# Kernel optimization log

Measured on AMD Instinct MI355X. Metric: run time of the kernel, lower is better.

The kernel has to match this reference:

```python
import jax, jax.numpy as jnp
import numpy as np

B, S, HID, NH, K = 4, 1500, 1024, 16, 64
DH = HID // NH  # 64


def _rel_bias(pos_emb, length):
    # pos_emb: [2K+1, d]; Shaw-style relative position embedding lookup -> [S, S, d]
    kk = (pos_emb.shape[0] - 1) // 2
    idx = jnp.arange(length)
    dist = jnp.clip(idx[None, :] - idx[:, None], -kk, kk) + kk
    return pos_emb[dist]


def setup_inputs() -> dict:
    key = jax.random.key(0)
    ks = jax.random.split(key, 12)
    sq = 1.0 / np.sqrt(HID)
    inp = {
        "query": jax.random.normal(ks[0], (B, S, HID), jnp.float32),
        "key": jax.random.normal(ks[1], (B, S, HID), jnp.float32),
        "value": jax.random.normal(ks[2], (B, S, HID), jnp.float32),
        # per-head QKV projections stacked over heads: [NH, HID, DH]
        "Wq": jax.random.normal(ks[3], (NH, HID, DH), jnp.float32) * sq,
        "bq": jnp.zeros((NH, DH), jnp.float32),
        "Wk": jax.random.normal(ks[4], (NH, HID, DH), jnp.float32) * sq,
        "bk": jnp.zeros((NH, DH), jnp.float32),
        "Wv": jax.random.normal(ks[5], (NH, HID, DH), jnp.float32) * sq,
        "bv": jnp.zeros((NH, DH), jnp.float32),
        # relative position tables [2K+1, DH]
        "pos_k": jax.random.normal(ks[6], (2 * K + 1, DH), jnp.float32) * 0.1,
        "pos_v": jax.random.normal(ks[7], (2 * K + 1, DH), jnp.float32) * 0.1,
        # output projection
        "W_fc": jax.random.normal(ks[8], (HID, HID), jnp.float32) * sq,
        "b_fc": jnp.zeros((HID,), jnp.float32),
    }
    return inp


def reference(query, key, value, Wq, bq, Wk, bk, Wv, bv, pos_k, pos_v, W_fc, b_fc):
    seq = query.shape[1]
    k_bias = _rel_bias(pos_k, seq)  # [S, S, DH]
    v_bias = _rel_bias(pos_v, seq)  # [S, S, DH]

    # batched per-head projections: [B, NH, S, DH]
    q = jnp.einsum('bsh,nhd->bnsd', query, Wq) + bq[None, :, None, :]
    k = jnp.einsum('bsh,nhd->bnsd', key, Wk) + bk[None, :, None, :]
    v = jnp.einsum('bsh,nhd->bnsd', value, Wv) + bv[None, :, None, :]

    attn_1 = jnp.einsum('bnqd,bnkd->bnqk', q, k)
    attn_2 = jnp.einsum('bnqd,qkd->bnqk', q, k_bias)  # Shaw relative key bias
    scores = (attn_1 + attn_2) / jnp.sqrt(jnp.float32(DH))
    w = jax.nn.softmax(scores, axis=-1)  # [B, NH, S, S]

    values_1 = jnp.einsum('bnqk,bnkd->bnqd', w, v)
    values_2 = jnp.einsum('bnqk,qkd->bnqd', w, v_bias)  # Shaw relative value bias
    heads = values_1 + values_2  # [B, NH, S, DH]

    # concat heads in head order -> [B, S, HID]
    hidden = jnp.transpose(heads, (0, 2, 1, 3)).reshape(query.shape[0], seq, -1)
    return hidden @ W_fc + b_fc
```

## Files before the change

kernel.cpp:

```cpp
#include <hip/hip_runtime.h>
#include <stdint.h>

typedef unsigned short u16;
typedef __attribute__((ext_vector_type(8))) short bf16x8;
typedef __attribute__((ext_vector_type(4))) float f32x4;

#define MFMA16(a, b, c) __builtin_amdgcn_mfma_f32_16x16x32_bf16(a, b, c, 0, 0, 0)

__device__ __forceinline__ u16 f2bf(float x) {
  union { float f; uint32_t u; } v; v.f = x;
  uint32_t r = (v.u + 0x7FFFu + ((v.u >> 16) & 1u)) >> 16;
  return (u16)r;
}
__device__ __forceinline__ float bf2f(u16 h) {
  union { uint32_t u; float f; } v; v.u = ((uint32_t)h) << 16; return v.f;
}
__device__ __forceinline__ uint cvt_pk_bf16(float a, float b) {
  uint r;
  asm("v_cvt_pk_bf16_f32 %0, %1, %2" : "=v"(r) : "v"(a), "v"(b));
  return r;
}
__device__ __forceinline__ void gll16(const void* g, void* s) {
  __builtin_amdgcn_global_load_lds((const __attribute__((address_space(1))) unsigned int*)g,
                                   (__attribute__((address_space(3))) unsigned int*)s, 16, 0, 0);
}


__global__ __launch_bounds__(256) void pack_x_kernel(const float* __restrict__ q,
                                                     const float* __restrict__ k,
                                                     const float* __restrict__ v,
                                                     u16* __restrict__ X) {
  const float* src = blockIdx.z == 0 ? q : (blockIdx.z == 1 ? k : v);
  u16* dst = X + (size_t)blockIdx.z * (6016UL * 1024UL);
  size_t idx = (size_t)blockIdx.x * 1024 + (size_t)threadIdx.x * 4;
  float4 f = *(const float4*)(src + idx);
  uint2 o;
  o.x = cvt_pk_bf16(f.x, f.y);
  o.y = cvt_pk_bf16(f.z, f.w);
  *(uint2*)(dst + idx) = o;
}

__global__ __launch_bounds__(256) void pack_w_kernel(const float* __restrict__ Wq,
                                                     const float* __restrict__ Wk,
                                                     const float* __restrict__ Wv,
                                                     const float* __restrict__ Wfc,
                                                     const float* __restrict__ bq,
                                                     const float* __restrict__ bk,
                                                     const float* __restrict__ bv,
                                                     const float* __restrict__ posk,
                                                     const float* __restrict__ posv,
                                                     u16* __restrict__ Wt,
                                                     u16* __restrict__ Wfct,
                                                     float* __restrict__ biascat,
                                                     u16* __restrict__ poskbf,
                                                     u16* __restrict__ posvT) {
  __shared__ float tile[64][65];
  const int bi = blockIdx.x;
  if (bi == 1024) {
    for (int i = threadIdx.x; i < 1024; i += 256) {
      biascat[i] = bq[i]; biascat[1024 + i] = bk[i]; biascat[2048 + i] = bv[i];
    }
    for (int i = threadIdx.x; i < 144 * 64; i += 256) {
      int r = i >> 6;
      poskbf[i] = (r < 129) ? f2bf(posk[i]) : (u16)0;
    }
    const int d = threadIdx.x & 63, rr = threadIdx.x >> 6;
#pragma unroll
    for (int j = 0; j < 34; ++j) {
      const int r = rr * 34 + j;
      posvT[d * 136 + r] = (r < 129) ? f2bf(posv[(size_t)r * 64 + d]) : (u16)0;
    }
    return;
  }
  const int r = threadIdx.x >> 2, c0 = (threadIdx.x & 3) * 16;
  const float* src;
  u16* outp;
  if (bi < 768) {
    const int z = bi >> 8, rem = bi & 255, n = rem >> 4, h0 = (rem & 15) * 64;
    const float* W = z == 0 ? Wq : (z == 1 ? Wk : Wv);
    src = W + (size_t)n * 65536 + (size_t)(h0 + r) * 64 + c0;
    outp = Wt + (size_t)z * (1024UL * 1024UL) + (size_t)(n * 64 + r) * 1024 + h0 + c0;
  } else {
    const int t = bi - 768;
    const int i0 = (t & 15) * 64, o0 = (t >> 4) * 64;
    src = Wfc + (size_t)(i0 + r) * 1024 + o0 + c0;
    outp = Wfct + (size_t)(o0 + r) * 1024 + i0 + c0;
  }
#pragma unroll
  for (int j = 0; j < 16; j += 4) {
    float4 f = *(const float4*)(src + j);
    tile[r][c0 + j] = f.x; tile[r][c0 + j + 1] = f.y;
    tile[r][c0 + j + 2] = f.z; tile[r][c0 + j + 3] = f.w;
  }
  __syncthreads();
#pragma unroll
  for (int j = 0; j < 16; ++j) outp[j] = f2bf(tile[c0 + j][r]);
}

__global__ __launch_bounds__(256) void vtrans_kernel(const u16* __restrict__ qkv,
                                                     u16* __restrict__ Vt) {
  const size_t ZS = 4UL * 16 * 1536 * 64;
  __shared__ u16 t[64][72];
  const int bh = blockIdx.x & 63, s0 = (blockIdx.x >> 6) * 64;
  const u16* src = qkv + 2 * ZS + (size_t)bh * (1536UL * 64UL) + (size_t)s0 * 64;
  const int r = threadIdx.x >> 2, c0 = (threadIdx.x & 3) * 16;
  *(uint4*)&t[r][c0]     = *(const uint4*)(src + (size_t)r * 64 + c0);
  *(uint4*)&t[r][c0 + 8] = *(const uint4*)(src + (size_t)r * 64 + c0 + 8);
  __syncthreads();
  uint4 a, bvec;
  uint tmp[8];
#pragma unroll
  for (int j = 0; j < 8; ++j)
    tmp[j] = (uint)t[c0 + 2 * j][r] | ((uint)t[c0 + 2 * j + 1][r] << 16);
  a.x = tmp[0]; a.y = tmp[1]; a.z = tmp[2]; a.w = tmp[3];
  bvec.x = tmp[4]; bvec.y = tmp[5]; bvec.z = tmp[6]; bvec.w = tmp[7];
  u16* dst = Vt + (size_t)(bh * 64 + r) * 1536 + s0 + c0;
  *(uint4*)dst = a;
  *(uint4*)(dst + 8) = bvec;
}

__global__ __launch_bounds__(256) void gemm_bt_kernel(
    const u16* __restrict__ Abase, long aStride,
    const u16* __restrict__ Bbase, long bStride,
    const float* __restrict__ biasBase, long biasStride,
    u16* __restrict__ outBF, float* __restrict__ outF, int mode) {
  const int z = blockIdx.z;
  const u16* A = Abase + (size_t)z * aStride;
  const u16* Bt = Bbase + (size_t)z * bStride;
  const float* bias = biasBase + (size_t)z * biasStride;
  __shared__ u16 As[128 * 32];
  __shared__ u16 Bs[128 * 32];
  const int tid = threadIdx.x, w = tid >> 6, lane = tid & 63;
  const int quad = lane >> 4, l16 = lane & 15;
  const int wm = w >> 1, wn = w & 1;
  const int m0 = blockIdx.y * 128, n0 = blockIdx.x * 128;
  const int srow = w * 16 + (lane >> 2);
  const int scol = (lane & 3) * 8;
  const u16* gA0 = A + (size_t)(m0 + srow) * 1024 + scol;
  const u16* gA1 = gA0 + 64UL * 1024;
  const u16* gB0 = Bt + (size_t)(n0 + srow) * 1024 + scol;
  const u16* gB1 = gB0 + 64UL * 1024;
  u16* lA0 = As + (w * 16) * 32;
  u16* lA1 = As + (64 + w * 16) * 32;
  u16* lB0 = Bs + (w * 16) * 32;
  u16* lB1 = Bs + (64 + w * 16) * 32;

  f32x4 acc[4][4];
  const f32x4 zf = {0.f, 0.f, 0.f, 0.f};
#pragma unroll
  for (int a = 0; a < 4; ++a)
#pragma unroll
    for (int b = 0; b < 4; ++b) acc[a][b] = zf;

  for (int kt = 0; kt < 32; ++kt) {
    const int k0 = kt * 32;
    gll16(gA0 + k0, lA0);
    gll16(gA1 + k0, lA1);
    gll16(gB0 + k0, lB0);
    gll16(gB1 + k0, lB1);
    __syncthreads();
    bf16x8 af[4], bfr[4];
#pragma unroll
    for (int f = 0; f < 4; ++f) {
      af[f]  = *(const bf16x8*)(As + (wm * 64 + f * 16 + l16) * 32 + quad * 8);
      bfr[f] = *(const bf16x8*)(Bs + (wn * 64 + f * 16 + l16) * 32 + quad * 8);
    }
#pragma unroll
    for (int fm = 0; fm < 4; ++fm)
#pragma unroll
      for (int fn = 0; fn < 4; ++fn)
        acc[fm][fn] = MFMA16(af[fm], bfr[fn], acc[fm][fn]);
    __syncthreads();
  }

  if (mode == 0) {
    const float scale = (z == 0) ? 0.125f : 1.0f;
    u16* out = outBF + (size_t)z * (4UL * 16 * 1536 * 64);
#pragma unroll
    for (int fm = 0; fm < 4; ++fm) {
#pragma unroll
      for (int i = 0; i < 4; ++i) {
        const int m = m0 + wm * 64 + fm * 16 + quad * 4 + i;
        if (m >= 6000) continue;
        const int bb = m / 1500;
        const int s = m - bb * 1500;
#pragma unroll
        for (int fn = 0; fn < 4; ++fn) {
          const int n = n0 + wn * 64 + fn * 16 + l16;
          const float vv = (acc[fm][fn][i] + bias[n]) * scale;
          const int h = n >> 6, d = n & 63;
          out[((size_t)(bb * 16 + h) * 1536 + s) * 64 + d] = f2bf(vv);
        }
      }
    }
  } else {
#pragma unroll
    for (int fm = 0; fm < 4; ++fm) {
#pragma unroll
      for (int i = 0; i < 4; ++i) {
        const int m = m0 + wm * 64 + fm * 16 + quad * 4 + i;
        if (m >= 6000) continue;
#pragma unroll
        for (int fn = 0; fn < 4; ++fn) {
          const int n = n0 + wn * 64 + fn * 16 + l16;
          outF[(size_t)m * 1024 + n] = acc[fm][fn][i] + bias[n];
        }
      }
    }
  }
}

__global__ __launch_bounds__(256) void attn_kernel(const u16* __restrict__ qkv,
                                                   const u16* __restrict__ Vt,
                                                   const u16* __restrict__ poskbf,
                                                   const u16* __restrict__ posvT,
                                                   const float* __restrict__ posv,
                                                   u16* __restrict__ hidden) {
  const size_t ZS = 4UL * 16 * 1536 * 64;
  __shared__ u16 qp_s[64 * 136];
  __shared__ u16 pb_s[64 * 136];
  __shared__ u16 kbuf[2][2048];
  __shared__ u16 vbuf[2][2048];

  const int tid = threadIdx.x;
  const int w = tid >> 6, lane = tid & 63, quad = lane >> 4, l16 = lane & 15;
  const int bi = blockIdx.x;
  const int bh = bi & 63;
  const int q0 = (bi >> 6) * 64, qw0 = q0 + w * 16;
  const int b = bh >> 4;
  const size_t sb = (size_t)bh * (1536UL * 64UL);
  const u16* Qp = qkv + sb;
  const u16* Kp = qkv + ZS + sb;
  const u16* Vtb = Vt + (size_t)bh * (64UL * 1536UL);
  u16* qp_row = qp_s + (w * 16 + l16) * 136;
  u16* pb_row = pb_s + (w * 16 + l16) * 136;

  const int r8 = lane >> 3, c8 = lane & 7;
  const int vr = lane >> 2, vc = lane & 3;
  const int kprow = ((( (w * 8 + r8) & 15) >> 2) * 8) + (((w * 8 + r8) >> 4) * 4) + ((w * 8 + r8) & 3);
  auto stageK = [&](int it, int buf) {
    const u16* src = Kp + (size_t)(it * 32 + kprow) * 64 + ((c8 ^ r8) * 8);
    gll16(src, &kbuf[buf][w * 512]);
  };
  auto stageV = [&](int it, int buf) {
    const u16* src = Vtb + (size_t)(w * 16 + vr) * 1536 + it * 32 + ((vc ^ ((vr >> 1) & 3)) * 8);
    gll16(src, &vbuf[buf][w * 512]);
  };

  {
    uint* pz = (uint*)(pb_s + w * 16 * 136);
    for (int i = lane; i < 1088; i += 64) pz[i] = 0u;
  }

  stageK(0, 0);
  stageV(0, 0);

  const u16* qptr = Qp + (size_t)(qw0 + l16) * 64 + quad * 8;
  const bf16x8 qB0 = *(const bf16x8*)qptr;
  const bf16x8 qB1 = *(const bf16x8*)(qptr + 32);

  const f32x4 zf = {0.f, 0.f, 0.f, 0.f};
#pragma unroll
  for (int nf = 0; nf < 9; ++nf) {
    const u16* bp = poskbf + (size_t)(nf * 16 + l16) * 64 + quad * 8;
    bf16x8 b0 = *(const bf16x8*)bp;
    bf16x8 b1 = *(const bf16x8*)(bp + 32);
    f32x4 c = zf;
    c = MFMA16(qB0, b0, c);
    c = MFMA16(qB1, b1, c);
    const int col = nf * 16 + l16;
    if (col < 136) {
#pragma unroll
      for (int i = 0; i < 4; ++i)
        qp_s[(w * 16 + quad * 4 + i) * 136 + col] = f2bf(c[i]);
    }
  }
  __syncthreads();

  const float L2E = 1.44269504f;
  const float M8 = -8.0f * L2E;
  const float eLow  = __builtin_fmaf(bf2f(qp_row[0]), L2E, M8);
  const float eHigh = __builtin_fmaf(bf2f(qp_row[128]), L2E, M8);

  f32x4 accf[4];
#pragma unroll
  for (int dc = 0; dc < 4; ++dc) accf[dc] = zf;
  float sSimple = 0.f, sLowSave = 0.f, sDall = 0.f, sD0 = 0.f, sD128 = 0.f;

  const int itLowEnd = (qw0 >= 95) ? (((qw0 - 95) >> 5) + 1) : 0;
  const int itHigh0 = (qw0 + 110) >> 5;
  const int dEnd = itHigh0 < 46 ? itHigh0 : 46;

  const int kswz = (quad ^ (l16 & 7)) * 8;
  const int kswz4 = ((quad + 4) ^ (l16 & 7)) * 8;
  const int vpos = (quad ^ ((l16 >> 1) & 3)) * 8;

  for (int it = 0; it < 47; ++it) {
    const int cur = it & 1;
    if (it < 46) { stageK(it + 1, cur ^ 1); stageV(it + 1, cur ^ 1); }

    if (it == itLowEnd) sLowSave = sSimple;
    const int phase = (it < itLowEnd) ? 0 : ((it >= 46) ? 1 : ((it < dEnd) ? 1 : 2));

    const u16* kb = kbuf[cur];
    bf16x8 ka00 = *(const bf16x8*)(kb + l16 * 64 + kswz);
    bf16x8 ka01 = *(const bf16x8*)(kb + l16 * 64 + kswz4);
    bf16x8 ka10 = *(const bf16x8*)(kb + (16 + l16) * 64 + kswz);
    bf16x8 ka11 = *(const bf16x8*)(kb + (16 + l16) * 64 + kswz4);
    const u16* vbse = vbuf[cur];
    bf16x8 vb0 = *(const bf16x8*)(vbse + l16 * 32 + vpos);
    bf16x8 vb1 = *(const bf16x8*)(vbse + (16 + l16) * 32 + vpos);
    bf16x8 vb2 = *(const bf16x8*)(vbse + (32 + l16) * 32 + vpos);
    bf16x8 vb3 = *(const bf16x8*)(vbse + (48 + l16) * 32 + vpos);

    float qb[2][4];
    if (phase == 1) {
      const int base = it * 32 + 64 - qw0 - l16 + quad * 8;
#pragma unroll
      for (int cg = 0; cg < 2; ++cg) {
#pragma unroll
        for (int i = 0; i < 4; ++i) {
          int delta = base + cg * 4 + i;
          delta = delta < 0 ? 0 : (delta > 128 ? 128 : delta);
          qb[cg][i] = bf2f(qp_row[delta]);
        }
      }
    }

    f32x4 cc[2];
    cc[0] = zf; cc[1] = zf;
    cc[0] = MFMA16(ka00, qB0, cc[0]);
    cc[0] = MFMA16(ka01, qB1, cc[0]);
    cc[1] = MFMA16(ka10, qB0, cc[1]);
    cc[1] = MFMA16(ka11, qB1, cc[1]);

    float pvv[2][4];
    if (phase != 1) {
      const float eB = (phase == 0) ? eLow : eHigh;
#pragma unroll
      for (int cg = 0; cg < 2; ++cg) {
#pragma unroll
        for (int i = 0; i < 4; ++i) {
          float p = __builtin_amdgcn_exp2f(__builtin_fmaf(cc[cg][i], L2E, eB));
          sSimple += p; pvv[cg][i] = p;
        }
      }
    } else {
      const int kc0 = it * 32;
#pragma unroll
      for (int cg = 0; cg < 2; ++cg) {
        const int krow0 = kc0 + quad * 8 + cg * 4;
        const int dbase = krow0 + 64 - qw0 - l16;
#pragma unroll
        for (int i = 0; i < 4; ++i) {
          int delta = dbase + i;
          delta = delta < 0 ? 0 : (delta > 128 ? 128 : delta);
          const float t = cc[cg][i] + qb[cg][i];
          float p = __builtin_amdgcn_exp2f(__builtin_fmaf(t, L2E, M8));
          if (krow0 + i >= 1500) p = 0.f;
          sDall += p;
          sD0   += (delta == 0)   ? p : 0.f;
          sD128 += (delta == 128) ? p : 0.f;
          pvv[cg][i] = p;
        }
        const uint pk01 = cvt_pk_bf16(pvv[cg][0], pvv[cg][1]);
        const uint pk23 = cvt_pk_bf16(pvv[cg][2], pvv[cg][3]);
        const u16 hb[4] = {(u16)pk01, (u16)(pk01 >> 16), (u16)pk23, (u16)(pk23 >> 16)};
#pragma unroll
        for (int i = 0; i < 4; ++i) {
          int delta = dbase + i;
          delta = delta < 0 ? 0 : (delta > 128 ? 128 : delta);
          if ((delta != 0) & (delta != 128)) pb_row[delta] = hb[i];
        }
      }
    }

    union { uint u[4]; bf16x8 v; } pa;
    pa.u[0] = cvt_pk_bf16(pvv[0][0], pvv[0][1]);
    pa.u[1] = cvt_pk_bf16(pvv[0][2], pvv[0][3]);
    pa.u[2] = cvt_pk_bf16(pvv[1][0], pvv[1][1]);
    pa.u[3] = cvt_pk_bf16(pvv[1][2], pvv[1][3]);

    accf[0] = MFMA16(pa.v, vb0, accf[0]);
    accf[1] = MFMA16(pa.v, vb1, accf[1]);
    accf[2] = MFMA16(pa.v, vb2, accf[2]);
    accf[3] = MFMA16(pa.v, vb3, accf[3]);

    __syncthreads();
  }

  const float sLow = sLowSave;
  const float sHigh = sSimple - sLowSave;
  float lpart = sSimple + sDall;
  float clow = sLow + sD0;
  float chigh = sHigh + sD128;
#pragma unroll
  for (int m = 16; m <= 32; m <<= 1) {
    lpart += __shfl_xor(lpart, m);
    clow  += __shfl_xor(clow, m);
    chigh += __shfl_xor(chigh, m);
  }
  const float linv = 1.0f / lpart;

  f32x4 o2[4];
#pragma unroll
  for (int dc = 0; dc < 4; ++dc) o2[dc] = zf;
  const u16* pbr = pb_s + (w * 16 + l16) * 136;
#pragma unroll
  for (int kk = 0; kk < 4; ++kk) {
    bf16x8 pa2 = *(const bf16x8*)(pbr + kk * 32 + quad * 8);
#pragma unroll
    for (int dc = 0; dc < 4; ++dc) {
      bf16x8 vb2r = *(const bf16x8*)(posvT + (size_t)(dc * 16 + l16) * 136 + kk * 32 + quad * 8);
      o2[dc] = MFMA16(pa2, vb2r, o2[dc]);
    }
  }

  float li[4], cl[4], ch[4];
#pragma unroll
  for (int i = 0; i < 4; ++i) {
    const int srcl = quad * 4 + i;
    li[i] = __shfl(linv, srcl);
    cl[i] = __shfl(clow, srcl);
    ch[i] = __shfl(chigh, srcl);
  }

#pragma unroll
  for (int dc = 0; dc < 4; ++dc) {
    const int d = dc * 16 + l16;
    const float pv0 = posv[d], pv1 = posv[128 * 64 + d];
#pragma unroll
    for (int i = 0; i < 4; ++i) {
      const int qg = qw0 + quad * 4 + i;
      if (qg < 1500) {
        const float val = (accf[dc][i] + o2[dc][i] + cl[i] * pv0 + ch[i] * pv1) * li[i];
        hidden[((size_t)(b * 1500 + qg)) * 1024 + (bh & 15) * 64 + d] = f2bf(val);
      }
    }
  }
}

extern "C" void kernel_launch(void* const* d_in, const int* in_sizes, int n_in,
                              void* d_out, int out_size, void* d_ws, size_t ws_size,
                              hipStream_t stream) {
  const float* query = (const float*)d_in[0];
  const float* key   = (const float*)d_in[1];
  const float* value = (const float*)d_in[2];
  const float* Wq = (const float*)d_in[3];
  const float* bq = (const float*)d_in[4];
  const float* Wk = (const float*)d_in[5];
  const float* bk = (const float*)d_in[6];
  const float* Wv = (const float*)d_in[7];
  const float* bv = (const float*)d_in[8];
  const float* posk = (const float*)d_in[9];
  const float* posv = (const float*)d_in[10];
  const float* Wfc = (const float*)d_in[11];
  const float* bfc = (const float*)d_in[12];
  float* out = (float*)d_out;

  char* p = (char*)d_ws;
  u16* X = (u16*)p;        p += 3UL * 6016 * 1024 * 2;
  u16* Wt = (u16*)p;       p += 3UL * 1024 * 1024 * 2;
  u16* Wfct = (u16*)p;     p += 1024UL * 1024 * 2;
  u16* poskbf = (u16*)p;   p += 144UL * 64 * 2;
  u16* posvT = (u16*)p;    p += 64UL * 136 * 2;
  float* biascat = (float*)p; p += 3UL * 1024 * 4;
  u16* qkv = (u16*)p;      p += 3UL * 4 * 16 * 1536 * 64 * 2;
  u16* hidden = X;
  u16* Vt = X + 6291456;

  pack_x_kernel<<<dim3(6000, 1, 3), 256, 0, stream>>>(query, key, value, X);
  pack_w_kernel<<<dim3(1025), 256, 0, stream>>>(Wq, Wk, Wv, Wfc, bq, bk, bv, posk, posv,
                                                Wt, Wfct, biascat, poskbf, posvT);

  gemm_bt_kernel<<<dim3(8, 47, 3), 256, 0, stream>>>(
      X, 6016L * 1024, Wt, 1024L * 1024, biascat, 1024L, qkv, nullptr, 0);

  vtrans_kernel<<<dim3(1536), 256, 0, stream>>>(qkv, Vt);

  attn_kernel<<<dim3(1536), 256, 0, stream>>>(qkv, Vt, poskbf, posvT, posv, hidden);

  gemm_bt_kernel<<<dim3(8, 47, 1), 256, 0, stream>>>(
      hidden, 0L, Wfct, 0L, bfc, 0L, nullptr, out, 1);
}
```

Before: 368.3 us.

## Load V tiles straight to registers with prefetch and shrink LDS rows to 128

The attention kernel drops the LDS double buffer for V. Each wave now loads its V fragments directly from global memory into registers, one iteration ahead. The qp/pb shared rows shrink from a 136 to a 128 stride, and the single column-128 relative-key value moves into a spare pb_s slot held in a register. This cuts LDS footprint and LDS traffic and may raise occupancy, but every wave now loads the whole V tile separately, which raises L2/global traffic. The power-of-two row stride may also add LDS bank conflicts.

```diff
diff --git a/kernel.cpp b/kernel.cpp
--- a/kernel.cpp
+++ b/kernel.cpp
@@ -217,10 +217,9 @@
                                                    const float* __restrict__ posv,
                                                    u16* __restrict__ hidden) {
   const size_t ZS = 4UL * 16 * 1536 * 64;
-  __shared__ u16 qp_s[64 * 136];
-  __shared__ u16 pb_s[64 * 136];
+  __shared__ u16 qp_s[64 * 128];
+  __shared__ u16 pb_s[64 * 128];
   __shared__ u16 kbuf[2][2048];
-  __shared__ u16 vbuf[2][2048];
 
   const int tid = threadIdx.x;
   const int w = tid >> 6, lane = tid & 63, quad = lane >> 4, l16 = lane & 15;
@@ -232,28 +231,28 @@
   const u16* Qp = qkv + sb;
   const u16* Kp = qkv + ZS + sb;
   const u16* Vtb = Vt + (size_t)bh * (64UL * 1536UL);
-  u16* qp_row = qp_s + (w * 16 + l16) * 136;
-  u16* pb_row = pb_s + (w * 16 + l16) * 136;
+  u16* qp_row = qp_s + (w * 16 + l16) * 128;
+  u16* pb_row = pb_s + (w * 16 + l16) * 128;
 
   const int r8 = lane >> 3, c8 = lane & 7;
-  const int vr = lane >> 2, vc = lane & 3;
   const int kprow = ((( (w * 8 + r8) & 15) >> 2) * 8) + (((w * 8 + r8) >> 4) * 4) + ((w * 8 + r8) & 3);
   auto stageK = [&](int it, int buf) {
     const u16* src = Kp + (size_t)(it * 32 + kprow) * 64 + ((c8 ^ r8) * 8);
     gll16(src, &kbuf[buf][w * 512]);
   };
-  auto stageV = [&](int it, int buf) {
-    const u16* src = Vtb + (size_t)(w * 16 + vr) * 1536 + it * 32 + ((vc ^ ((vr >> 1) & 3)) * 8);
-    gll16(src, &vbuf[buf][w * 512]);
-  };
 
   {
-    uint* pz = (uint*)(pb_s + w * 16 * 136);
-    for (int i = lane; i < 1088; i += 64) pz[i] = 0u;
+    uint* pz = (uint*)(pb_s + w * 16 * 128);
+    for (int i = lane; i < 1024; i += 64) pz[i] = 0u;
   }
 
   stageK(0, 0);
-  stageV(0, 0);
+
+  const u16* vBase = Vtb + (size_t)l16 * 1536 + quad * 8;
+  bf16x8 vb0 = *(const bf16x8*)(vBase);
+  bf16x8 vb1 = *(const bf16x8*)(vBase + 16 * 1536);
+  bf16x8 vb2 = *(const bf16x8*)(vBase + 32 * 1536);
+  bf16x8 vb3 = *(const bf16x8*)(vBase + 48 * 1536);
 
   const u16* qptr = Qp + (size_t)(qw0 + l16) * 64 + quad * 8;
   const bf16x8 qB0 = *(const bf16x8*)qptr;
@@ -268,19 +267,25 @@
     f32x4 c = zf;
     c = MFMA16(qB0, b0, c);
     c = MFMA16(qB1, b1, c);
-    const int col = nf * 16 + l16;
-    if (col < 136) {
+    if (nf < 8) {
+      const int col = nf * 16 + l16;
 #pragma unroll
       for (int i = 0; i < 4; ++i)
-        qp_s[(w * 16 + quad * 4 + i) * 136 + col] = f2bf(c[i]);
+        qp_s[(w * 16 + quad * 4 + i) * 128 + col] = f2bf(c[i]);
+    } else if (l16 == 0) {
+#pragma unroll
+      for (int i = 0; i < 4; ++i)
+        pb_s[(w * 16 + quad * 4 + i) * 128] = f2bf(c[i]);
     }
   }
   __syncthreads();
 
   const float L2E = 1.44269504f;
   const float M8 = -8.0f * L2E;
+  const float qpHigh = bf2f(pb_row[0]);
   const float eLow  = __builtin_fmaf(bf2f(qp_row[0]), L2E, M8);
-  const float eHigh = __builtin_fmaf(bf2f(qp_row[128]), L2E, M8);
+  const float eHigh = __builtin_fmaf(qpHigh, L2E, M8);
+  pb_row[0] = 0;
 
   f32x4 accf[4];
 #pragma unroll
@@ -293,11 +298,16 @@
 
   const int kswz = (quad ^ (l16 & 7)) * 8;
   const int kswz4 = ((quad + 4) ^ (l16 & 7)) * 8;
-  const int vpos = (quad ^ ((l16 >> 1) & 3)) * 8;
 
   for (int it = 0; it < 47; ++it) {
     const int cur = it & 1;
-    if (it < 46) { stageK(it + 1, cur ^ 1); stageV(it + 1, cur ^ 1); }
+    if (it < 46) stageK(it + 1, cur ^ 1);
+
+    const u16* vn = vBase + (it + 1) * 32;
+    bf16x8 nv0 = *(const bf16x8*)(vn);
+    bf16x8 nv1 = *(const bf16x8*)(vn + 16 * 1536);
+    bf16x8 nv2 = *(const bf16x8*)(vn + 32 * 1536);
+    bf16x8 nv3 = *(const bf16x8*)(vn + 48 * 1536);
 
     if (it == itLowEnd) sLowSave = sSimple;
     const int phase = (it < itLowEnd) ? 0 : ((it >= 46) ? 1 : ((it < dEnd) ? 1 : 2));
@@ -307,11 +317,6 @@
     bf16x8 ka01 = *(const bf16x8*)(kb + l16 * 64 + kswz4);
     bf16x8 ka10 = *(const bf16x8*)(kb + (16 + l16) * 64 + kswz);
     bf16x8 ka11 = *(const bf16x8*)(kb + (16 + l16) * 64 + kswz4);
-    const u16* vbse = vbuf[cur];
-    bf16x8 vb0 = *(const bf16x8*)(vbse + l16 * 32 + vpos);
-    bf16x8 vb1 = *(const bf16x8*)(vbse + (16 + l16) * 32 + vpos);
-    bf16x8 vb2 = *(const bf16x8*)(vbse + (32 + l16) * 32 + vpos);
-    bf16x8 vb3 = *(const bf16x8*)(vbse + (48 + l16) * 32 + vpos);
 
     float qb[2][4];
     if (phase == 1) {
@@ -322,7 +327,8 @@
         for (int i = 0; i < 4; ++i) {
           int delta = base + cg * 4 + i;
           delta = delta < 0 ? 0 : (delta > 128 ? 128 : delta);
-          qb[cg][i] = bf2f(qp_row[delta]);
+          const float qv = bf2f(qp_row[delta & 127]);
+          qb[cg][i] = (delta == 128) ? qpHigh : qv;
         }
       }
     }
@@ -386,6 +392,8 @@
     accf[2] = MFMA16(pa.v, vb2, accf[2]);
     accf[3] = MFMA16(pa.v, vb3, accf[3]);
 
+    vb0 = nv0; vb1 = nv1; vb2 = nv2; vb3 = nv3;
+
     __syncthreads();
   }
 
@@ -405,7 +413,7 @@
   f32x4 o2[4];
 #pragma unroll
   for (int dc = 0; dc < 4; ++dc) o2[dc] = zf;
-  const u16* pbr = pb_s + (w * 16 + l16) * 136;
+  const u16* pbr = pb_s + (w * 16 + l16) * 128;
 #pragma unroll
   for (int kk = 0; kk < 4; ++kk) {
     bf16x8 pa2 = *(const bf16x8*)(pbr + kk * 32 + quad * 8);
```

New measurement: 438.2 us. 1.19x slower.
